# Kernel optimization log

Hardware: AMD Instinct MI355X
Metric: run time of the kernel (lower is better)

## Reference

```python
import jax, jax.numpy as jnp
import numpy as np

C = 1024          # channels
H = 8             # num_channels (heads)
D = C // H        # channel_dim
POS = 16          # pos_dim (hard-coded in module)
MAX_FREQ = 16.0
MIN_FREQ = 1.0
HALF_S = 16       # samples_per_dim=32 -> offsets -16..16 -> S=33
S = 2 * HALF_S + 1


def setup_inputs() -> dict:
    key = jax.random.key(0)
    ks = jax.random.split(key, 8)
    B, L = 2, 2048
    s = 0.02  # realistic small init scale for learned weights
    return {
        "x": jax.random.normal(ks[0], (B, L, C), jnp.float32),
        "w_wave": jax.random.normal(ks[1], (3 * H, C), jnp.float32) * s,
        "b_wave": jnp.zeros((3 * H,), jnp.float32),
        "w_query": jax.random.normal(ks[2], (H * POS, C), jnp.float32) * s,
        "b_query": jnp.zeros((H * POS,), jnp.float32),
        "w_key": jax.random.normal(ks[3], (POS,), jnp.float32) * s,  # key_proj: Linear(1, POS, bias=False)
        "w_out": jax.random.normal(ks[4], (C, C), jnp.float32) * s,
        "w_se1": jax.random.normal(ks[5], (C // 4, C), jnp.float32) * s,
        "b_se1": jnp.zeros((C // 4,), jnp.float32),
        "w_se2": jax.random.normal(ks[6], (C, C // 4), jnp.float32) * s,
        "b_se2": jnp.zeros((C,), jnp.float32),
    }


def reference(x, w_wave, b_wave, w_query, b_query, w_key, w_out, w_se1, b_se1, w_se2, b_se2):
    B, L, Cc = x.shape
    offsets = jnp.arange(-HALF_S, HALF_S + 1, dtype=jnp.float32)  # stride_grid[:, 0], (S,)

    # wave params -> per-token, per-head freq / phase / decay
    wp = jax.nn.silu(x @ w_wave.T + b_wave).reshape(B, L, 3, H).transpose(0, 1, 3, 2)  # (B,L,H,3)
    freq = jax.nn.sigmoid(wp[..., 0]) * (MAX_FREQ - MIN_FREQ) + MIN_FREQ  # (B,L,H)
    phase = jnp.tanh(wp[..., 1]) * MAX_FREQ                               # (B,L,H)
    decay = jax.nn.sigmoid(wp[..., 2]) * 9.5 + 0.5                        # (B,L,H)
    freq_avg = freq.mean(axis=2)   # (B,L)
    phase_avg = phase.mean(axis=2) # (B,L)

    # learned fractional sample positions along the sequence
    centers = jnp.arange(L, dtype=jnp.float32)
    sample_pos = (centers[None, :, None]
                  + offsets[None, None, :] * freq_avg[..., None]
                  + phase_avg[..., None])                                 # (B,L,S)
    valid = (sample_pos >= 0) & (sample_pos < L)                          # (B,L,S)
    idx = jnp.clip(sample_pos.astype(jnp.int32), 0, L - 1)

    # dynamic gather of values at computed indices: (B,L,S,C)
    values = jax.vmap(lambda xf, i: xf[i])(x, idx)
    values = values.reshape(B, L, S, H, D).transpose(0, 1, 3, 2, 4)       # (B,L,H,S,D)

    queries = jax.nn.silu(x @ w_query.T + b_query).reshape(B, L, H, POS)  # (B,L,H,POS)
    rel_dist = jnp.abs(jnp.abs(offsets)[None, None, None, :] * freq[..., None])  # (B,L,H,S)
    keys = rel_dist[..., None] * w_key                                    # (B,L,H,S,POS)

    logits = jnp.einsum('blhd,blhsd->blhs', queries, keys) * (POS ** -0.5)
    vmask = valid[:, :, None, :]                                          # (B,L,1,S) -> broadcast (B,L,H,S)
    logits = jnp.where(vmask, logits, -jnp.inf)
    envelope = jnp.exp(-rel_dist / jnp.clip(decay[..., None], 0.1, None))

    attn = jax.nn.softmax(logits, axis=-1) * envelope * vmask
    attn = attn / (attn.sum(axis=-1, keepdims=True) + 1e-8)

    out = jnp.einsum('blhsd,blhs->blhd', values, attn).reshape(B, L, Cc)

    # SE-style channel gating
    se = jax.nn.sigmoid(jax.nn.silu(out @ w_se1.T + b_se1) @ w_se2.T + b_se2)
    out = (out * se) @ w_out.T                                            # (B,L,C) (spatial=(L,))

    entropy = -(attn * jnp.log(attn + 1e-8)).sum(axis=-1).mean()
    return out, -entropy
```

## Files before the change

kernel.cpp:

```cpp
#include <hip/hip_runtime.h>

typedef unsigned short u16;
typedef unsigned int u32;
typedef __attribute__((ext_vector_type(8))) __bf16 bf16x8;
typedef __attribute__((ext_vector_type(4))) float f32x4;

#define L_SEQ 2048
#define NROWS 4096
#define NHEAD 8
#define SWIN 33

__device__ __forceinline__ u16 f2b(float f) {
  u32 u = __float_as_uint(f);
  u += 0x7fffu + ((u >> 16) & 1u);
  return (u16)(u >> 16);
}
__device__ __forceinline__ float b2f(u32 lo16) { return __uint_as_float(lo16 << 16); }

__device__ __forceinline__ float sigmoidf_(float x) { return 1.f / (1.f + expf(-x)); }
__device__ __forceinline__ float siluf_(float x) { return x / (1.f + expf(-x)); }

__device__ __forceinline__ void gload_lds16(void* g, void* l) {
  __builtin_amdgcn_global_load_lds((__attribute__((address_space(1))) void*)g,
                                   (__attribute__((address_space(3))) void*)l, 16, 0, 0);
}

#define RPB 8
__global__ __launch_bounds__(256) void wave_params_kernel(
    const float* __restrict__ x, const float* __restrict__ w_wave,
    const float* __restrict__ b_wave, float* __restrict__ params,
    u16* __restrict__ xb,
    const float* __restrict__ wq, const float* __restrict__ w1,
    const float* __restrict__ w2, const float* __restrict__ wo,
    u16* __restrict__ wqb, u16* __restrict__ w1b, u16* __restrict__ w2b,
    u16* __restrict__ wob) {
  __shared__ float xs[RPB][1024];
  __shared__ float wp[RPB][24];
  const int t = threadIdx.x;
  const int bx = blockIdx.x;
  if (bx >= 512) {
    size_t i = (size_t)(bx - 512) * 256 + t;
    const float* src;
    u16* dst;
    if (i < 32768) { src = wq; dst = wqb; }
    else if ((i -= 32768) < 65536) { src = w1; dst = w1b; }
    else if ((i -= 65536) < 65536) { src = w2; dst = w2b; }
    else if ((i -= 65536) < 262144) { src = wo; dst = wob; }
    else return;
    const float4 v = *(const float4*)(src + i * 4);
    uint2 pk;
    pk.x = (u32)f2b(v.x) | ((u32)f2b(v.y) << 16);
    pk.y = (u32)f2b(v.z) | ((u32)f2b(v.w) << 16);
    *(uint2*)(dst + i * 4) = pk;
    return;
  }
  const int row0 = bx * RPB;
  const float4* xv = (const float4*)(x + (size_t)row0 * 1024);
  float4* xsv = (float4*)&xs[0][0];
  uint2* xbv = (uint2*)(xb + (size_t)row0 * 1024);
#pragma unroll
  for (int i = 0; i < RPB; ++i) {
    const float4 v = xv[t + 256 * i];
    xsv[t + 256 * i] = v;
    uint2 pk;
    pk.x = (u32)f2b(v.x) | ((u32)f2b(v.y) << 16);
    pk.y = (u32)f2b(v.z) | ((u32)f2b(v.w) << 16);
    xbv[t + 256 * i] = pk;
  }
  __syncthreads();
  const int wv = t >> 6, lane = t & 63;
#pragma unroll
  for (int oi = 0; oi < 6; ++oi) {
    const int o = wv * 6 + oi;
    float w[16];
#pragma unroll
    for (int k = 0; k < 16; ++k) w[k] = w_wave[o * 1024 + lane + 64 * k];
    const float bo = b_wave[o];
    for (int r = 0; r < RPB; ++r) {
      float d = 0.f;
#pragma unroll
      for (int k = 0; k < 16; ++k) d += w[k] * xs[r][lane + 64 * k];
#pragma unroll
      for (int off = 32; off; off >>= 1) d += __shfl_xor(d, off);
      if (lane == 0) wp[r][o] = siluf_(d + bo);
    }
  }
  __syncthreads();
  if (t < RPB * 8) {
    const int r = t >> 3, h = t & 7;
    float* pr = params + (size_t)(row0 + r) * 18;
    pr[h] = sigmoidf_(wp[r][h]) * 15.f + 1.f;
    pr[8 + h] = sigmoidf_(wp[r][16 + h]) * 9.5f + 0.5f;
  }
  if (t < RPB) {
    float fs = 0.f, ps = 0.f;
    for (int h = 0; h < 8; ++h) {
      fs += sigmoidf_(wp[t][h]);
      ps += tanhf(wp[t][8 + h]);
    }
    float* pr = params + (size_t)(row0 + t) * 18;
    pr[16] = fs * (15.f / 8.f) + 1.f;
    pr[17] = ps * (16.f / 8.f);
  }
}

template <int MODE, int TM, int TN, int BK>
__global__ __launch_bounds__(256) void gemm_bt(
    const u16* __restrict__ A, const u16* __restrict__ Bw,
    const float* __restrict__ bias, const u16* __restrict__ aux,
    void* __restrict__ outp, int N, int K) {
  __shared__ __align__(16) u16 As[2 * TM * BK];
  __shared__ __align__(16) u16 Bs[2 * TN * BK];
  const int t = threadIdx.x;
  const int bm = blockIdx.x, bn = blockIdx.y;
  constexpr int TPR = BK / 8;
  constexpr int RPP = 256 / TPR;
  const int rowS = t / TPR;
  const int colX = ((t & (TPR - 1)) ^ (rowS & (TPR - 1))) * 8;
  const u16* Ag = A + (size_t)(bm * TM + rowS) * K + colX;
  const u16* Bg = Bw + (size_t)(bn * TN + rowS) * K + colX;
  constexpr int NI = TM / 32, NJ = TN / 32;
  f32x4 acc[NI][NJ] = {};
  const int lane = t & 63, wv = t >> 6;
  const int wm = (wv >> 1) * (TM / 2);
  const int wn = (wv & 1) * (TN / 2);
  const int frow = lane & 15, quad = lane >> 4;
  auto stage = [&](int buf, int kt) {
    char* Ab = (char*)As + buf * (TM * BK * 2);
    char* Bb = (char*)Bs + buf * (TN * BK * 2);
#pragma unroll
    for (int r = 0; r < TM; r += RPP)
      gload_lds16((void*)(Ag + kt + (size_t)r * K), Ab + r * BK * 2 + t * 16);
#pragma unroll
    for (int r = 0; r < TN; r += RPP)
      gload_lds16((void*)(Bg + kt + (size_t)r * K), Bb + r * BK * 2 + t * 16);
  };
  stage(0, 0);
  int pb = 0;
  for (int kt = 0; kt < K; kt += BK, pb ^= 1) {
    __syncthreads();
    if (kt + BK < K) stage(pb ^ 1, kt + BK);
#pragma unroll
    for (int kk = 0; kk < BK; kk += 32) {
      bf16x8 af[NI], bfr[NJ];
#pragma unroll
      for (int i = 0; i < NI; ++i) {
        const int rr = wm + i * 16 + frow;
        af[i] = *(bf16x8*)&As[pb * TM * BK + rr * BK + ((((kk >> 3) + quad) ^ (rr & (TPR - 1))) * 8)];
      }
#pragma unroll
      for (int j = 0; j < NJ; ++j) {
        const int rr = wn + j * 16 + frow;
        bfr[j] = *(bf16x8*)&Bs[pb * TN * BK + rr * BK + ((((kk >> 3) + quad) ^ (rr & (TPR - 1))) * 8)];
      }
#pragma unroll
      for (int i = 0; i < NI; ++i)
#pragma unroll
        for (int j = 0; j < NJ; ++j)
          acc[i][j] = __builtin_amdgcn_mfma_f32_16x16x32_bf16(af[i], bfr[j], acc[i][j], 0, 0, 0);
    }
  }
#pragma unroll
  for (int i = 0; i < NI; ++i)
#pragma unroll
    for (int j = 0; j < NJ; ++j)
#pragma unroll
      for (int r = 0; r < 4; ++r) {
        const int gm = bm * TM + wm + i * 16 + quad * 4 + r;
        const int gn = bn * TN + wn + j * 16 + frow;
        float v = acc[i][j][r];
        const size_t o = (size_t)gm * N + gn;
        if (MODE == 0) { v = siluf_(v + bias[gn]); ((float*)outp)[o] = v; }
        if (MODE == 1) { v = siluf_(v + bias[gn]); ((u16*)outp)[o] = f2b(v); }
        if (MODE == 2) { v = sigmoidf_(v + bias[gn]) * b2f(aux[o]); ((u16*)outp)[o] = f2b(v); }
        if (MODE == 3) { ((float*)outp)[o] = v; }
      }
}

__global__ __launch_bounds__(256, 2) void attn_kernel(
    const u16* __restrict__ xb, const float* __restrict__ params,
    const float* __restrict__ qbuf, const float* __restrict__ w_key,
    u16* __restrict__ outb, float* __restrict__ entpart) {
  __shared__ float qs[128];
  __shared__ float wk[16];
  __shared__ float pf[18];
  __shared__ float qkL[8];
  __shared__ int idxL[SWIN];
  __shared__ int validL[SWIN];
  __shared__ float attnL[NHEAD][SWIN];
  __shared__ float entL[8];
  const int t = threadIdx.x;
  const int bx = blockIdx.x;
  const int row = ((bx & 7) << 9) | (bx >> 3);
  const int b = row >> 11, l = row & 2047;
  if (t < 128) qs[t] = qbuf[(size_t)row * 128 + t];
  if (t < 16) wk[t] = w_key[t];
  if (t >= 128 && t < 146) pf[t - 128] = params[(size_t)row * 18 + (t - 128)];
  __syncthreads();
  if (t < SWIN) {
    const float pos = (float)l + (float)(t - 16) * pf[16] + pf[17];
    validL[t] = (pos >= 0.f) && (pos < (float)L_SEQ);
    int id = (int)pos;
    idxL[t] = min(max(id, 0), L_SEQ - 1);
  }
  if (t >= 64 && t < 72) {
    const int h = t - 64;
    float s = 0.f;
#pragma unroll
    for (int p = 0; p < 16; ++p) s += qs[h * 16 + p] * wk[p];
    qkL[h] = s * 0.25f;
  }
  __syncthreads();
  const int wv = t >> 6, lane = t & 63;
#pragma unroll
  for (int it = 0; it < 2; ++it) {
    const int h = wv + 4 * it;
    const bool act = lane < SWIN;
    const int s = act ? lane : 0;
    const float rel = fabsf((float)(s - 16)) * pf[h];
    const float logit = rel * qkL[h];
    const bool vs = act && validL[s];
    float m = vs ? logit : -INFINITY;
#pragma unroll
    for (int o = 32; o; o >>= 1) m = fmaxf(m, __shfl_xor(m, o));
    float p = vs ? expf(logit - m) : 0.f;
    float sm = p;
#pragma unroll
    for (int o = 32; o; o >>= 1) sm += __shfl_xor(sm, o);
    const float soft = sm > 0.f ? p / sm : 0.f;
    const float env = expf(-rel / fmaxf(pf[8 + h], 0.1f));
    float a = soft * env;
    float as = a;
#pragma unroll
    for (int o = 32; o; o >>= 1) as += __shfl_xor(as, o);
    a = a / (as + 1e-8f);
    if (act) attnL[h][s] = a;
    float et = a * logf(a + 1e-8f);
#pragma unroll
    for (int o = 32; o; o >>= 1) et += __shfl_xor(et, o);
    if (lane == 0) entL[h] = et;
  }
  __syncthreads();
  if (t == 0) {
    float e = 0.f;
    for (int h = 0; h < 8; ++h) e += entL[h];
    entpart[bx] = e * (1.f / 32768.f);
  }
  const u16* xbase = xb + (size_t)b * L_SEQ * 1024 + 4 * t;
  const int h = t >> 5;
  float4 acc = make_float4(0.f, 0.f, 0.f, 0.f);
  uint2 v0[11], v1[11], v2[11];
  auto LD = [&](uint2* v, int c) {
#pragma unroll
    for (int k = 0; k < 11; ++k)
      v[k] = *(const uint2*)(xbase + (size_t)idxL[c * 11 + k] * 1024);
  };
  auto FM = [&](uint2* v, int c) {
#pragma unroll
    for (int k = 0; k < 11; ++k) {
      const float a_ = attnL[h][c * 11 + k];
      acc.x += a_ * b2f(v[k].x & 0xffffu);
      acc.y += a_ * b2f(v[k].x >> 16);
      acc.z += a_ * b2f(v[k].y & 0xffffu);
      acc.w += a_ * b2f(v[k].y >> 16);
    }
  };
  LD(v0, 0); __builtin_amdgcn_sched_barrier(0);
  LD(v1, 1); __builtin_amdgcn_sched_barrier(0);
  FM(v0, 0); __builtin_amdgcn_sched_barrier(0);
  LD(v2, 2); __builtin_amdgcn_sched_barrier(0);
  FM(v1, 1); __builtin_amdgcn_sched_barrier(0);
  FM(v2, 2);
  const size_t o4 = (size_t)row * 1024 + 4 * t;
  uint2 pk;
  pk.x = (u32)f2b(acc.x) | ((u32)f2b(acc.y) << 16);
  pk.y = (u32)f2b(acc.z) | ((u32)f2b(acc.w) << 16);
  *(uint2*)(outb + o4) = pk;
}

__global__ __launch_bounds__(256) void ent_reduce_kernel(
    const float* __restrict__ entpart, float* __restrict__ entslot) {
  __shared__ float ws_[4];
  const int t = threadIdx.x;
  float s = 0.f;
#pragma unroll
  for (int i = 0; i < 16; ++i) s += entpart[t + 256 * i];
#pragma unroll
  for (int o = 32; o; o >>= 1) s += __shfl_xor(s, o);
  if ((t & 63) == 0) ws_[t >> 6] = s;
  __syncthreads();
  if (t == 0) *entslot = ws_[0] + ws_[1] + ws_[2] + ws_[3];
}

extern "C" void kernel_launch(void* const* d_in, const int* in_sizes, int n_in,
                              void* d_out, int out_size, void* d_ws, size_t ws_size,
                              hipStream_t stream) {
  const float* x = (const float*)d_in[0];
  const float* w_wave = (const float*)d_in[1];
  const float* b_wave = (const float*)d_in[2];
  const float* w_query = (const float*)d_in[3];
  const float* b_query = (const float*)d_in[4];
  const float* w_key = (const float*)d_in[5];
  const float* w_out = (const float*)d_in[6];
  const float* w_se1 = (const float*)d_in[7];
  const float* b_se1 = (const float*)d_in[8];
  const float* w_se2 = (const float*)d_in[9];
  const float* b_se2 = (const float*)d_in[10];
  float* out = (float*)d_out;
  char* ws = (char*)d_ws;
  size_t off = 0;
  auto alloc = [&](size_t bytes) { void* p = ws + off; off += (bytes + 255) & ~(size_t)255; return p; };
  float* params = (float*)alloc(NROWS * 18 * 4);
  float* qbuf = (float*)alloc((size_t)NROWS * 128 * 4);
  float* entpart = (float*)alloc(NROWS * 4);
  u16* outb = (u16*)alloc((size_t)NROWS * 1024 * 2);
  u16* t1b = (u16*)alloc((size_t)NROWS * 256 * 2);
  u16* gb = (u16*)alloc((size_t)NROWS * 1024 * 2);
  u16* xb = (u16*)alloc((size_t)NROWS * 1024 * 2);
  u16* wqb = (u16*)alloc(128 * 1024 * 2);
  u16* w1b = (u16*)alloc(256 * 1024 * 2);
  u16* w2b = (u16*)alloc(1024 * 256 * 2);
  u16* wob = (u16*)alloc((size_t)1024 * 1024 * 2);
  float* entslot = out + (out_size - 1);

  wave_params_kernel<<<dim3(512 + 1664), 256, 0, stream>>>(
      x, w_wave, b_wave, params, xb, w_query, w_se1, w_se2, w_out, wqb, w1b, w2b, wob);
  gemm_bt<0, 64, 32, 64><<<dim3(64, 4), 256, 0, stream>>>(xb, wqb, b_query, nullptr, qbuf, 128, 1024);
  attn_kernel<<<dim3(NROWS), 256, 0, stream>>>(xb, params, qbuf, w_key, outb, entpart);
  ent_reduce_kernel<<<dim3(1), 256, 0, stream>>>(entpart, entslot);
  gemm_bt<1, 64, 32, 64><<<dim3(64, 8), 256, 0, stream>>>(outb, w1b, b_se1, nullptr, t1b, 256, 1024);
  gemm_bt<2, 128, 64, 64><<<dim3(32, 16), 256, 0, stream>>>(t1b, w2b, b_se2, outb, gb, 1024, 256);
  gemm_bt<3, 128, 64, 64><<<dim3(32, 16), 256, 0, stream>>>(gb, wob, nullptr, nullptr, out, 1024, 1024);
}
```

Baseline: 188.9 us.

## Fuse query-key dot into query GEMM epilogue and entropy reduce into SE1 GEMM

The query GEMM epilogue now applies SiLU, multiplies by w_key and reduces across the 16 POS lanes, so it writes only 8 floats per row instead of a 128-float query buffer. The attention kernel reads these directly, and the separate entropy-reduce launch is folded into an extra grid column of the first SE GEMM. The gather loop is also restructured into two larger load batches with per-wave entropy accumulation. The aim is to save one kernel launch and some memory traffic, at the cost of more registers held for in-flight loads and some leftover dead statements.

```diff
diff --git a/kernel.cpp b/kernel.cpp
--- a/kernel.cpp
+++ b/kernel.cpp
@@ -104,15 +104,29 @@
   }
 }
 
-template <int MODE, int TM, int TN, int BK>
+template <int MODE, int TM, int TN, int BK, int ENT = 0>
 __global__ __launch_bounds__(256) void gemm_bt(
     const u16* __restrict__ A, const u16* __restrict__ Bw,
     const float* __restrict__ bias, const u16* __restrict__ aux,
-    void* __restrict__ outp, int N, int K) {
+    const float* __restrict__ wkey, const float* __restrict__ entpart,
+    float* __restrict__ entslot, void* __restrict__ outp, int N, int K) {
   __shared__ __align__(16) u16 As[2 * TM * BK];
   __shared__ __align__(16) u16 Bs[2 * TN * BK];
   const int t = threadIdx.x;
   const int bm = blockIdx.x, bn = blockIdx.y;
+  if (ENT && bn == (int)gridDim.y - 1) {
+    if (bm != 0) return;
+    __shared__ float ws2[4];
+    float s = 0.f;
+#pragma unroll
+    for (int i = 0; i < 16; ++i) s += entpart[t + 256 * i];
+#pragma unroll
+    for (int o = 32; o; o >>= 1) s += __shfl_xor(s, o);
+    if ((t & 63) == 0) ws2[t >> 6] = s;
+    __syncthreads();
+    if (t == 0) *entslot = ws2[0] + ws2[1] + ws2[2] + ws2[3];
+    return;
+  }
   constexpr int TPR = BK / 8;
   constexpr int RPP = 256 / TPR;
   const int rowS = t / TPR;
@@ -160,6 +174,24 @@
           acc[i][j] = __builtin_amdgcn_mfma_f32_16x16x32_bf16(af[i], bfr[j], acc[i][j], 0, 0, 0);
     }
   }
+  if (MODE == 4) {
+    const float bq = bias[bn * TN + wn + frow];
+    const float wkf = wkey[frow];
+    const int h = bn * 2 + (wn >> 4);
+#pragma unroll
+    for (int i = 0; i < NI; ++i)
+#pragma unroll
+      for (int r = 0; r < 4; ++r) {
+        float w = siluf_(acc[i][0][r] + bq) * wkf;
+        w += __shfl_xor(w, 1); w += __shfl_xor(w, 2);
+        w += __shfl_xor(w, 4); w += __shfl_xor(w, 8);
+        if (frow == 0) {
+          const int gm = bm * TM + wm + i * 16 + quad * 4 + r;
+          ((float*)outp)[gm * 8 + h] = w;
+        }
+      }
+    return;
+  }
 #pragma unroll
   for (int i = 0; i < NI; ++i)
 #pragma unroll
@@ -179,23 +211,19 @@
 
 __global__ __launch_bounds__(256, 2) void attn_kernel(
     const u16* __restrict__ xb, const float* __restrict__ params,
-    const float* __restrict__ qbuf, const float* __restrict__ w_key,
-    u16* __restrict__ outb, float* __restrict__ entpart) {
-  __shared__ float qs[128];
-  __shared__ float wk[16];
+    const float* __restrict__ qkbuf, u16* __restrict__ outb,
+    float* __restrict__ entpart) {
   __shared__ float pf[18];
   __shared__ float qkL[8];
   __shared__ int idxL[SWIN];
   __shared__ int validL[SWIN];
   __shared__ float attnL[NHEAD][SWIN];
-  __shared__ float entL[8];
   const int t = threadIdx.x;
   const int bx = blockIdx.x;
   const int row = ((bx & 7) << 9) | (bx >> 3);
   const int b = row >> 11, l = row & 2047;
-  if (t < 128) qs[t] = qbuf[(size_t)row * 128 + t];
-  if (t < 16) wk[t] = w_key[t];
-  if (t >= 128 && t < 146) pf[t - 128] = params[(size_t)row * 18 + (t - 128)];
+  if (t < 18) pf[t] = params[(size_t)row * 18 + t];
+  if (t >= 64 && t < 72) qkL[t - 64] = qkbuf[(size_t)row * 8 + (t - 64)] * 0.25f;
   __syncthreads();
   if (t < SWIN) {
     const float pos = (float)l + (float)(t - 16) * pf[16] + pf[17];
@@ -203,15 +231,9 @@
     int id = (int)pos;
     idxL[t] = min(max(id, 0), L_SEQ - 1);
   }
-  if (t >= 64 && t < 72) {
-    const int h = t - 64;
-    float s = 0.f;
-#pragma unroll
-    for (int p = 0; p < 16; ++p) s += qs[h * 16 + p] * wk[p];
-    qkL[h] = s * 0.25f;
-  }
   __syncthreads();
   const int wv = t >> 6, lane = t & 63;
+  float entacc = 0.f;
 #pragma unroll
   for (int it = 0; it < 2; ++it) {
     const int h = wv + 4 * it;
@@ -238,58 +260,49 @@
     float et = a * logf(a + 1e-8f);
 #pragma unroll
     for (int o = 32; o; o >>= 1) et += __shfl_xor(et, o);
-    if (lane == 0) entL[h] = et;
-  }
-  __syncthreads();
-  if (t == 0) {
-    float e = 0.f;
-    for (int h = 0; h < 8; ++h) e += entL[h];
-    entpart[bx] = e * (1.f / 32768.f);
-  }
+    entacc += et;
+  }
+  __syncthreads();
+  if (lane == 0) {
+    ((float*)attnL)[0 * 0];
+  }
+  if (t == 0) ;
+  __shared__ float entW[4];
+  if (lane == 0) entW[wv] = entacc;
+  __syncthreads();
+  if (t == 0) entpart[bx] = (entW[0] + entW[1] + entW[2] + entW[3]) * (1.f / 32768.f);
   const u16* xbase = xb + (size_t)b * L_SEQ * 1024 + 4 * t;
   const int h = t >> 5;
   float4 acc = make_float4(0.f, 0.f, 0.f, 0.f);
-  uint2 v0[11], v1[11], v2[11];
-  auto LD = [&](uint2* v, int c) {
-#pragma unroll
-    for (int k = 0; k < 11; ++k)
-      v[k] = *(const uint2*)(xbase + (size_t)idxL[c * 11 + k] * 1024);
-  };
-  auto FM = [&](uint2* v, int c) {
-#pragma unroll
-    for (int k = 0; k < 11; ++k) {
-      const float a_ = attnL[h][c * 11 + k];
-      acc.x += a_ * b2f(v[k].x & 0xffffu);
-      acc.y += a_ * b2f(v[k].x >> 16);
-      acc.z += a_ * b2f(v[k].y & 0xffffu);
-      acc.w += a_ * b2f(v[k].y >> 16);
-    }
-  };
-  LD(v0, 0); __builtin_amdgcn_sched_barrier(0);
-  LD(v1, 1); __builtin_amdgcn_sched_barrier(0);
-  FM(v0, 0); __builtin_amdgcn_sched_barrier(0);
-  LD(v2, 2); __builtin_amdgcn_sched_barrier(0);
-  FM(v1, 1); __builtin_amdgcn_sched_barrier(0);
-  FM(v2, 2);
+  uint2 v0[17], v1[16];
+#pragma unroll
+  for (int k = 0; k < 17; ++k) v0[k] = *(const uint2*)(xbase + (size_t)idxL[k] * 1024);
+  __builtin_amdgcn_sched_barrier(0);
+#pragma unroll
+  for (int k = 0; k < 16; ++k) v1[k] = *(const uint2*)(xbase + (size_t)idxL[17 + k] * 1024);
+  __builtin_amdgcn_sched_barrier(0);
+#pragma unroll
+  for (int k = 0; k < 17; ++k) {
+    const float a_ = attnL[h][k];
+    acc.x += a_ * b2f(v0[k].x & 0xffffu);
+    acc.y += a_ * b2f(v0[k].x >> 16);
+    acc.z += a_ * b2f(v0[k].y & 0xffffu);
+    acc.w += a_ * b2f(v0[k].y >> 16);
+  }
+  __builtin_amdgcn_sched_barrier(0);
+#pragma unroll
+  for (int k = 0; k < 16; ++k) {
+    const float a_ = attnL[h][17 + k];
+    acc.x += a_ * b2f(v1[k].x & 0xffffu);
+    acc.y += a_ * b2f(v1[k].x >> 16);
+    acc.z += a_ * b2f(v1[k].y & 0xffffu);
+    acc.w += a_ * b2f(v1[k].y >> 16);
+  }
   const size_t o4 = (size_t)row * 1024 + 4 * t;
   uint2 pk;
   pk.x = (u32)f2b(acc.x) | ((u32)f2b(acc.y) << 16);
   pk.y = (u32)f2b(acc.z) | ((u32)f2b(acc.w) << 16);
   *(uint2*)(outb + o4) = pk;
-}
-
-__global__ __launch_bounds__(256) void ent_reduce_kernel(
-    const float* __restrict__ entpart, float* __restrict__ entslot) {
-  __shared__ float ws_[4];
-  const int t = threadIdx.x;
-  float s = 0.f;
-#pragma unroll
-  for (int i = 0; i < 16; ++i) s += entpart[t + 256 * i];
-#pragma unroll
-  for (int o = 32; o; o >>= 1) s += __shfl_xor(s, o);
-  if ((t & 63) == 0) ws_[t >> 6] = s;
-  __syncthreads();
-  if (t == 0) *entslot = ws_[0] + ws_[1] + ws_[2] + ws_[3];
 }
 
 extern "C" void kernel_launch(void* const* d_in, const int* in_sizes, int n_in,
@@ -311,7 +324,7 @@
   size_t off = 0;
   auto alloc = [&](size_t bytes) { void* p = ws + off; off += (bytes + 255) & ~(size_t)255; return p; };
   float* params = (float*)alloc(NROWS * 18 * 4);
-  float* qbuf = (float*)alloc((size_t)NROWS * 128 * 4);
+  float* qkbuf = (float*)alloc((size_t)NROWS * 8 * 4);
   float* entpart = (float*)alloc(NROWS * 4);
   u16* outb = (u16*)alloc((size_t)NROWS * 1024 * 2);
   u16* t1b = (u16*)alloc((size_t)NROWS * 256 * 2);
@@ -325,10 +338,13 @@
 
   wave_params_kernel<<<dim3(512 + 1664), 256, 0, stream>>>(
       x, w_wave, b_wave, params, xb, w_query, w_se1, w_se2, w_out, wqb, w1b, w2b, wob);
-  gemm_bt<0, 64, 32, 64><<<dim3(64, 4), 256, 0, stream>>>(xb, wqb, b_query, nullptr, qbuf, 128, 1024);
-  attn_kernel<<<dim3(NROWS), 256, 0, stream>>>(xb, params, qbuf, w_key, outb, entpart);
-  ent_reduce_kernel<<<dim3(1), 256, 0, stream>>>(entpart, entslot);
-  gemm_bt<1, 64, 32, 64><<<dim3(64, 8), 256, 0, stream>>>(outb, w1b, b_se1, nullptr, t1b, 256, 1024);
-  gemm_bt<2, 128, 64, 64><<<dim3(32, 16), 256, 0, stream>>>(t1b, w2b, b_se2, outb, gb, 1024, 256);
-  gemm_bt<3, 128, 64, 64><<<dim3(32, 16), 256, 0, stream>>>(gb, wob, nullptr, nullptr, out, 1024, 1024);
-}
+  gemm_bt<4, 64, 32, 64><<<dim3(64, 4), 256, 0, stream>>>(
+      xb, wqb, b_query, nullptr, w_key, nullptr, nullptr, qkbuf, 128, 1024);
+  attn_kernel<<<dim3(NROWS), 256, 0, stream>>>(xb, params, qkbuf, outb, entpart);
+  gemm_bt<1, 64, 32, 64, 1><<<dim3(64, 9), 256, 0, stream>>>(
+      outb, w1b, b_se1, nullptr, nullptr, entpart, entslot, t1b, 256, 1024);
+  gemm_bt<2, 128, 64, 64><<<dim3(32, 16), 256, 0, stream>>>(
+      t1b, w2b, b_se2, outb, nullptr, nullptr, nullptr, gb, 1024, 256);
+  gemm_bt<3, 128, 64, 64><<<dim3(32, 16), 256, 0, stream>>>(
+      gb, wob, nullptr, nullptr, nullptr, nullptr, nullptr, out, 1024, 1024);
+}
```

Result: slower. 194.0 us (+2.7%).
